# Kernel tuning notes

Hardware: AMD Instinct MI355X
Metric: run time of the kernel (lower is better)

The kernel has to match this reference:

```python
import jax, jax.numpy as jnp
import numpy as np


def setup_inputs() -> dict:
    key = jax.random.key(0)
    ks = jax.random.split(key, 14)
    B, S, C, R = 4, 2048, 1024, 4
    s = 0.02
    inp = {
        "hidden_states": jax.random.normal(ks[0], (B, S, C), jnp.float32),
        "Wq": jax.random.normal(ks[1], (C, C), jnp.float32) * s,
        "Wk": jax.random.normal(ks[2], (C, C), jnp.float32) * s,
        "Wv": jax.random.normal(ks[3], (C, C), jnp.float32) * s,
        "Wo": jax.random.normal(ks[4], (C, C), jnp.float32) * s,
        "bo": jnp.zeros((C,), jnp.float32),
        "q_down": jax.random.normal(ks[5], (R, C), jnp.float32) * (1.0 / R),
        "q_up": jnp.zeros((C, R), jnp.float32) + jax.random.normal(ks[6], (C, R), jnp.float32) * s,
        "k_down": jax.random.normal(ks[7], (R, C), jnp.float32) * (1.0 / R),
        "k_up": jax.random.normal(ks[8], (C, R), jnp.float32) * s,
        "v_down": jax.random.normal(ks[9], (R, C), jnp.float32) * (1.0 / R),
        "v_up": jax.random.normal(ks[10], (C, R), jnp.float32) * s,
        "o_down": jax.random.normal(ks[11], (R, C), jnp.float32) * (1.0 / R),
        "o_up": jax.random.normal(ks[12], (C, R), jnp.float32) * s,
        "num_heads": 16,
    }
    return inp


def _lora_linear(x, W, down, up, scale):
    # base Linear (no bias) + lora_scale * up(down(x))
    base = jnp.einsum("bsc,oc->bso", x, W)
    low = jnp.einsum("bsc,rc->bsr", x, down)
    return base + scale * jnp.einsum("bsr,or->bso", low, up)


def reference(hidden_states, Wq, Wk, Wv, Wo, bo,
              q_down, q_up, k_down, k_up, v_down, v_up, o_down, o_up,
              num_heads):
    B, S, C = hidden_states.shape
    H = num_heads
    D = C // H
    lora_scale = 1.0

    q = _lora_linear(hidden_states, Wq, q_down, q_up, lora_scale)
    k = _lora_linear(hidden_states, Wk, k_down, k_up, lora_scale)
    v = _lora_linear(hidden_states, Wv, v_down, v_up, lora_scale)

    # head_to_batch_dim: [B,S,C] -> [B,H,S,D]
    q = q.reshape(B, S, H, D).transpose(0, 2, 1, 3)
    k = k.reshape(B, S, H, D).transpose(0, 2, 1, 3)
    v = v.reshape(B, S, H, D).transpose(0, 2, 1, 3)

    scale = 1.0 / jnp.sqrt(jnp.asarray(D, hidden_states.dtype))
    scores = jnp.einsum("bhsd,bhtd->bhst", q, k) * scale  # [B,H,S,S]
    probs = jax.nn.softmax(scores, axis=-1)
    out = jnp.einsum("bhst,bhtd->bhsd", probs, v)

    # batch_to_head_dim: [B,H,S,D] -> [B,S,C]
    out = out.transpose(0, 2, 1, 3).reshape(B, S, C)

    out = _lora_linear(out, Wo, o_down, o_up, lora_scale) + bo
    return out
```

## Files before the change

kernel.cpp:

```cpp
#include <hip/hip_runtime.h>
#include <stdint.h>

typedef __attribute__((ext_vector_type(8))) short short8;
typedef __attribute__((ext_vector_type(4))) float f32x4;

typedef const unsigned int __attribute__((address_space(1))) gu32;
typedef unsigned int __attribute__((address_space(3))) lu32;

__device__ __forceinline__ float bf2f(unsigned short u) {
  union { unsigned int i; float f; } v; v.i = ((unsigned int)u) << 16; return v.f;
}
__device__ __forceinline__ unsigned short f2bf(float f) {
  union { float f; unsigned int i; } v; v.f = f;
  unsigned int r = v.i + 0x7FFFu + ((v.i >> 16) & 1u);
  return (unsigned short)(r >> 16);
}
__device__ __forceinline__ float fexp2(float x) {
  float r; asm("v_exp_f32 %0, %1" : "=v"(r) : "v"(x)); return r;
}
__device__ __forceinline__ unsigned int cvtpk(float lo, float hi) {
  unsigned int r;
  asm("v_cvt_pk_bf16_f32 %0, %1, %2" : "=v"(r) : "v"(lo), "v"(hi));
  return r;
}

__global__ __launch_bounds__(256) void fold_w(
    const float* __restrict__ Wq, const float* __restrict__ Wk,
    const float* __restrict__ Wv, const float* __restrict__ Wo,
    const float* __restrict__ qd, const float* __restrict__ qu,
    const float* __restrict__ kd, const float* __restrict__ ku,
    const float* __restrict__ vd, const float* __restrict__ vu,
    const float* __restrict__ od, const float* __restrict__ ou,
    unsigned short* __restrict__ Wqkv, unsigned short* __restrict__ Wob)
{
  int idx = blockIdx.x * 256 + threadIdx.x;
  int sel = idx >> 18;
  int rem = (idx & 0x3FFFF) * 4;
  int o = rem >> 10, c = rem & 1023;
  const float *W, *up, *dn;
  if (sel == 0)      { W = Wq; up = qu; dn = qd; }
  else if (sel == 1) { W = Wk; up = ku; dn = kd; }
  else if (sel == 2) { W = Wv; up = vu; dn = vd; }
  else               { W = Wo; up = ou; dn = od; }
  float4 wv = *(const float4*)&W[rem];
  float a0 = wv.x, a1 = wv.y, a2 = wv.z, a3 = wv.w;
  #pragma unroll
  for (int r = 0; r < 4; r++) {
    float u = up[o * 4 + r];
    float4 dv = *(const float4*)&dn[r * 1024 + c];
    a0 += u * dv.x; a1 += u * dv.y; a2 += u * dv.z; a3 += u * dv.w;
  }
  unsigned long long pk = (unsigned long long)f2bf(a0) |
                          ((unsigned long long)f2bf(a1) << 16) |
                          ((unsigned long long)f2bf(a2) << 32) |
                          ((unsigned long long)f2bf(a3) << 48);
  if (sel < 3) *(unsigned long long*)&Wqkv[sel * 1048576 + rem] = pk;
  else         *(unsigned long long*)&Wob[rem] = pk;
}

__global__ __launch_bounds__(256) void cvt_x(const float* __restrict__ X,
                                             unsigned short* __restrict__ Xb)
{
  int i = (blockIdx.x * 256 + threadIdx.x) * 4;
  float4 v = *(const float4*)&X[i];
  unsigned short o0 = f2bf(v.x), o1 = f2bf(v.y), o2 = f2bf(v.z), o3 = f2bf(v.w);
  unsigned long long pk = (unsigned long long)o0 | ((unsigned long long)o1 << 16) |
                          ((unsigned long long)o2 << 32) | ((unsigned long long)o3 << 48);
  *(unsigned long long*)&Xb[i] = pk;
}

template <int OUTF>
__global__ __launch_bounds__(256) void gemm_bt(
    const unsigned short* __restrict__ A, const unsigned short* __restrict__ B,
    unsigned short* __restrict__ Cb, float* __restrict__ Cf,
    const float* __restrict__ bias, int M, int N, int K)
{
  __shared__ unsigned short smA[3][128 * 32];
  __shared__ unsigned short smB[3][128 * 32];
  const int tid = threadIdx.x;
  const int w = tid >> 6, lane = tid & 63;
  const int g = lane >> 4, lr = lane & 15;
  const int m0 = blockIdx.y * 128, n0 = blockIdx.x * 128;
  const int srow = lane >> 2;
  const int scol = (lane & 3) * 8;
  const unsigned short* gA = A + (size_t)(m0 + w * 16 + srow) * K + scol;
  const unsigned short* gB = B + (size_t)(n0 + w * 16 + srow) * K + scol;
  f32x4 acc[4][4] = {};
  const int wr = (w >> 1) * 64, wc = (w & 1) * 64;

  auto stage = [&](int buf, int k0) {
    #pragma unroll
    for (int i = 0; i < 2; i++) {
      __builtin_amdgcn_global_load_lds((gu32*)(gA + (size_t)i * 64 * K + k0),
          (lu32*)&smA[buf][(i * 64 + w * 16) * 32], 16, 0, 0);
      __builtin_amdgcn_global_load_lds((gu32*)(gB + (size_t)i * 64 * K + k0),
          (lu32*)&smB[buf][(i * 64 + w * 16) * 32], 16, 0, 0);
    }
  };
  auto compute = [&](int buf) {
    short8 a[4], b[4];
    #pragma unroll
    for (int mi = 0; mi < 4; mi++) a[mi] = *(const short8*)&smA[buf][(wr + mi * 16 + lr) * 32 + g * 8];
    #pragma unroll
    for (int ni = 0; ni < 4; ni++) b[ni] = *(const short8*)&smB[buf][(wc + ni * 16 + lr) * 32 + g * 8];
    #pragma unroll
    for (int mi = 0; mi < 4; mi++)
      #pragma unroll
      for (int ni = 0; ni < 4; ni++)
        acc[mi][ni] = __builtin_amdgcn_mfma_f32_16x16x32_bf16(a[mi], b[ni], acc[mi][ni], 0, 0, 0);
  };

  const int nt = K / 32;
  stage(0, 0);
  stage(1, 32);
  int cur = 0;
  for (int t = 0; t + 2 < nt; ++t) {
    asm volatile("s_waitcnt vmcnt(4)" ::: "memory");
    __builtin_amdgcn_sched_barrier(0);
    __builtin_amdgcn_s_barrier();
    __builtin_amdgcn_sched_barrier(0);
    int nb = (cur == 0) ? 2 : cur - 1;
    stage(nb, (t + 2) * 32);
    compute(cur);
    asm volatile("s_waitcnt lgkmcnt(0)" ::: "memory");
    __builtin_amdgcn_sched_barrier(0);
    cur = (cur == 2) ? 0 : cur + 1;
  }
  asm volatile("s_waitcnt vmcnt(4)" ::: "memory");
  __builtin_amdgcn_sched_barrier(0);
  __builtin_amdgcn_s_barrier();
  __builtin_amdgcn_sched_barrier(0);
  compute(cur);
  asm volatile("s_waitcnt lgkmcnt(0)" ::: "memory");
  __builtin_amdgcn_sched_barrier(0);
  cur = (cur == 2) ? 0 : cur + 1;
  asm volatile("s_waitcnt vmcnt(0)" ::: "memory");
  __builtin_amdgcn_sched_barrier(0);
  __builtin_amdgcn_s_barrier();
  __builtin_amdgcn_sched_barrier(0);
  compute(cur);

  #pragma unroll
  for (int mi = 0; mi < 4; mi++) {
    #pragma unroll
    for (int ni = 0; ni < 4; ni++) {
      int col = n0 + wc + ni * 16 + lr;
      #pragma unroll
      for (int j = 0; j < 4; j++) {
        int row = m0 + wr + mi * 16 + g * 4 + j;
        if (OUTF == 0) Cb[(size_t)row * N + col] = f2bf(acc[mi][ni][j]);
        else           Cf[(size_t)row * N + col] = acc[mi][ni][j] + bias[col];
      }
    }
  }
}

__global__ __launch_bounds__(256) void prep_kv(
    const unsigned short* __restrict__ QKV,
    unsigned short* __restrict__ Kswz, unsigned short* __restrict__ VTs)
{
  __shared__ unsigned short vt[64 * 72];
  int bh = blockIdx.x;
  int st = blockIdx.y;
  int b = bh >> 4, h = bh & 15;
  int s0 = st * 64;
  int tid = threadIdx.x;
  #pragma unroll
  for (int i = 0; i < 2; i++) {
    int idx = tid + i * 256;
    int r = idx >> 3, gch = idx & 7;
    size_t rowg = (size_t)(b * 2048 + s0 + r) * 3072;
    short8 kv = *(const short8*)&QKV[rowg + 1024 + h * 64 + gch * 8];
    int gout = gch ^ (r & 7);
    *(short8*)&Kswz[(size_t)(bh * 2048 + s0 + r) * 64 + gout * 8] = kv;
    short8 vv = *(const short8*)&QKV[rowg + 2048 + h * 64 + gch * 8];
    *(short8*)&vt[r * 72 + gch * 8] = vv;
  }
  __syncthreads();
  #pragma unroll
  for (int i = 0; i < 2; i++) {
    int idx = tid + i * 256;
    int d = idx >> 3, gp = idx & 7;
    int gs = gp ^ (d & 7);
    short8 o;
    #pragma unroll
    for (int j = 0; j < 8; j++) o[j] = (short)vt[(gs * 8 + j) * 72 + d];
    *(short8*)&VTs[(size_t)(bh * 64 + d) * 2048 + s0 + gp * 8] = o;
  }
}

__global__ __launch_bounds__(512, 4) void attn(
    const unsigned short* __restrict__ QKV,
    const unsigned short* __restrict__ Kswz,
    const unsigned short* __restrict__ VTs,
    unsigned short* __restrict__ O)
{
  __shared__ unsigned short smK[3][64 * 64];
  __shared__ unsigned short smV[3][64 * 64];
  __shared__ unsigned short smP[8][32 * 64];
  int bh = blockIdx.x, qb = blockIdx.y;
  int b = bh >> 4, h = bh & 15;
  int tid = threadIdx.x, w = tid >> 6, lane = tid & 63;
  int g = lane >> 4, lr = lane & 15;
  int q0 = qb * 256 + w * 32;
  const size_t kbse = (size_t)bh * 2048 * 64;
  const size_t vbse = (size_t)bh * 64 * 2048;
  const int srow8 = lane >> 3;
  const int sc8 = (lane & 7) * 8;

  auto stage = [&](int buf, int n0) {
    const unsigned short* gk = &Kswz[kbse + (size_t)(n0 + w * 8 + srow8) * 64 + sc8];
    __builtin_amdgcn_global_load_lds((gu32*)gk, (lu32*)&smK[buf][(w * 8) * 64], 16, 0, 0);
    const unsigned short* gv = &VTs[vbse + (size_t)(w * 8 + srow8) * 2048 + n0 + sc8];
    __builtin_amdgcn_global_load_lds((gu32*)gv, (lu32*)&smV[buf][(w * 8) * 64], 16, 0, 0);
  };

  const float SC = 0.125f * 1.44269504f;
  short8 bq[2][2];
  #pragma unroll
  for (int qf = 0; qf < 2; qf++)
    #pragma unroll
    for (int ks = 0; ks < 2; ks++) {
      short8 v = *(const short8*)&QKV[(size_t)(b * 2048 + q0 + qf * 16 + lr) * 3072 +
                                      h * 64 + ks * 32 + g * 8];
      #pragma unroll
      for (int j = 0; j < 4; j++) {
        float f0 = bf2f((unsigned short)v[2 * j]) * SC;
        float f1 = bf2f((unsigned short)v[2 * j + 1]) * SC;
        ((unsigned int*)&v)[j] = cvtpk(f0, f1);
      }
      bq[qf][ks] = v;
    }

  short8 vones;
  #pragma unroll
  for (int j = 0; j < 8; j++) vones[j] = (short)0x3F80;

  f32x4 acc_o[2][4] = {};
  f32x4 acc_l[2] = {};

  asm volatile("s_waitcnt vmcnt(0)" ::: "memory");
  __builtin_amdgcn_sched_barrier(0);
  stage(0, 0);
  stage(1, 64);

  auto compute = [&](int buf) {
    const unsigned short* K_ = smK[buf];
    const unsigned short* V_ = smV[buf];
    f32x4 s[4][2] = {};
    __builtin_amdgcn_s_setprio(1);
    #pragma unroll
    for (int nf = 0; nf < 4; nf++) {
      int row = nf * 16 + lr;
      #pragma unroll
      for (int ks = 0; ks < 2; ks++) {
        int eo = (ks * 64 + g * 16) ^ ((row & 7) << 4);
        short8 ak = *(const short8*)&K_[row * 64 + (eo >> 1)];
        #pragma unroll
        for (int qf = 0; qf < 2; qf++)
          s[nf][qf] = __builtin_amdgcn_mfma_f32_16x16x32_bf16(ak, bq[qf][ks], s[nf][qf], 0, 0, 0);
      }
    }
    __builtin_amdgcn_s_setprio(0);

    #pragma unroll
    for (int qf = 0; qf < 2; qf++) {
      int q = qf * 16 + lr;
      #pragma unroll
      for (int nf = 0; nf < 4; nf++) {
        float p0 = fexp2(s[nf][qf][0]);
        float p1 = fexp2(s[nf][qf][1]);
        float p2 = fexp2(s[nf][qf][2]);
        float p3 = fexp2(s[nf][qf][3]);
        uint2 pw;
        pw.x = cvtpk(p0, p1);
        pw.y = cvtpk(p2, p3);
        int eo = ((nf * 16 + g * 4) * 2) ^ ((q & 7) << 4);
        *(uint2*)&smP[w][q * 64 + (eo >> 1)] = pw;
      }
    }

    __builtin_amdgcn_s_setprio(1);
    #pragma unroll
    for (int ks = 0; ks < 2; ks++) {
      short8 ap[2];
      #pragma unroll
      for (int mq = 0; mq < 2; mq++) {
        int q = mq * 16 + lr;
        int eo = (ks * 64 + g * 16) ^ ((q & 7) << 4);
        ap[mq] = *(const short8*)&smP[w][q * 64 + (eo >> 1)];
        acc_l[mq] = __builtin_amdgcn_mfma_f32_16x16x32_bf16(ap[mq], vones, acc_l[mq], 0, 0, 0);
      }
      #pragma unroll
      for (int df = 0; df < 4; df++) {
        int d = df * 16 + lr;
        int eo = (ks * 64 + g * 16) ^ ((d & 7) << 4);
        short8 bv = *(const short8*)&V_[d * 64 + (eo >> 1)];
        #pragma unroll
        for (int mq = 0; mq < 2; mq++)
          acc_o[mq][df] = __builtin_amdgcn_mfma_f32_16x16x32_bf16(ap[mq], bv, acc_o[mq][df], 0, 0, 0);
      }
    }
    __builtin_amdgcn_s_setprio(0);
  };

  int cur = 0;
  for (int t = 0; t + 2 < 32; ++t) {
    asm volatile("s_waitcnt vmcnt(2)" ::: "memory");
    __builtin_amdgcn_sched_barrier(0);
    __builtin_amdgcn_s_barrier();
    __builtin_amdgcn_sched_barrier(0);
    int nb = (cur == 0) ? 2 : cur - 1;
    stage(nb, (t + 2) * 64);
    compute(cur);
    asm volatile("s_waitcnt lgkmcnt(0)" ::: "memory");
    __builtin_amdgcn_sched_barrier(0);
    cur = (cur == 2) ? 0 : cur + 1;
  }
  asm volatile("s_waitcnt vmcnt(2)" ::: "memory");
  __builtin_amdgcn_sched_barrier(0);
  __builtin_amdgcn_s_barrier();
  __builtin_amdgcn_sched_barrier(0);
  compute(cur);
  asm volatile("s_waitcnt lgkmcnt(0)" ::: "memory");
  __builtin_amdgcn_sched_barrier(0);
  cur = (cur == 2) ? 0 : cur + 1;
  asm volatile("s_waitcnt vmcnt(0)" ::: "memory");
  __builtin_amdgcn_sched_barrier(0);
  __builtin_amdgcn_s_barrier();
  __builtin_amdgcn_sched_barrier(0);
  compute(cur);

  #pragma unroll
  for (int mq = 0; mq < 2; mq++)
    #pragma unroll
    for (int j = 0; j < 4; j++) {
      float inv = 1.0f / acc_l[mq][j];
      #pragma unroll
      for (int df = 0; df < 4; df++) {
        int row = b * 2048 + q0 + mq * 16 + g * 4 + j;
        int col = h * 64 + df * 16 + lr;
        O[(size_t)row * 1024 + col] = f2bf(acc_o[mq][df][j] * inv);
      }
    }
}

extern "C" void kernel_launch(void* const* d_in, const int* in_sizes, int n_in,
                              void* d_out, int out_size, void* d_ws, size_t ws_size,
                              hipStream_t stream) {
  const float* X  = (const float*)d_in[0];
  const float* Wq = (const float*)d_in[1];
  const float* Wk = (const float*)d_in[2];
  const float* Wv = (const float*)d_in[3];
  const float* Wo = (const float*)d_in[4];
  const float* bo = (const float*)d_in[5];
  const float* qd = (const float*)d_in[6];
  const float* qu = (const float*)d_in[7];
  const float* kd = (const float*)d_in[8];
  const float* ku = (const float*)d_in[9];
  const float* vd = (const float*)d_in[10];
  const float* vu = (const float*)d_in[11];
  const float* od = (const float*)d_in[12];
  const float* ou = (const float*)d_in[13];

  char* ws = (char*)d_ws;
  unsigned short* Wqkv = (unsigned short*)(ws);
  unsigned short* Wob  = (unsigned short*)(ws + 6291456);
  unsigned short* Xb   = (unsigned short*)(ws + 8388608);
  unsigned short* QKV  = (unsigned short*)(ws + 25165824);
  unsigned short* Kswz = (unsigned short*)(ws + 75497472);
  unsigned short* VTs  = (unsigned short*)(ws + 92274688);

  fold_w<<<4096, 256, 0, stream>>>(Wq, Wk, Wv, Wo, qd, qu, kd, ku, vd, vu, od, ou, Wqkv, Wob);
  cvt_x<<<8192, 256, 0, stream>>>(X, Xb);
  gemm_bt<0><<<dim3(24, 64), 256, 0, stream>>>(Xb, Wqkv, QKV, nullptr, nullptr, 8192, 3072, 1024);
  prep_kv<<<dim3(64, 32), 256, 0, stream>>>(QKV, Kswz, VTs);
  attn<<<dim3(64, 8), 512, 0, stream>>>(QKV, Kswz, VTs, Xb);
  gemm_bt<1><<<dim3(8, 64), 256, 0, stream>>>(Xb, Wob, nullptr, (float*)d_out, bo, 8192, 1024, 1024);
}
```

Before: 193.7 us.

## Fuse K swizzle into QKV GEMM epilogue, enlarge GEMM tiles, merge prep kernels

The X conversion and weight folding now run in a single launch. The QKV GEMM epilogue writes the K section directly in the swizzled per-head layout, so the separate K copy drops out of the prep kernel, which now only transposes V. Both GEMMs move to 256x128 tiles with 512 threads and an XCD-aware 1D block mapping, for better operand reuse and L2 locality. The trade-off is that K is now written as scattered 2-byte stores from the epilogue, and larger tiles mean fewer blocks per GEMM.

```diff
diff --git a/kernel.cpp b/kernel.cpp
--- a/kernel.cpp
+++ b/kernel.cpp
@@ -24,7 +24,8 @@
   return r;
 }
 
-__global__ __launch_bounds__(256) void fold_w(
+__global__ __launch_bounds__(256) void prep_in(
+    const float* __restrict__ X, unsigned short* __restrict__ Xb,
     const float* __restrict__ Wq, const float* __restrict__ Wk,
     const float* __restrict__ Wv, const float* __restrict__ Wo,
     const float* __restrict__ qd, const float* __restrict__ qu,
@@ -33,7 +34,17 @@
     const float* __restrict__ od, const float* __restrict__ ou,
     unsigned short* __restrict__ Wqkv, unsigned short* __restrict__ Wob)
 {
-  int idx = blockIdx.x * 256 + threadIdx.x;
+  if (blockIdx.x < 8192) {
+    int i = (blockIdx.x * 256 + threadIdx.x) * 4;
+    float4 v = *(const float4*)&X[i];
+    unsigned long long pk = (unsigned long long)f2bf(v.x) |
+                            ((unsigned long long)f2bf(v.y) << 16) |
+                            ((unsigned long long)f2bf(v.z) << 32) |
+                            ((unsigned long long)f2bf(v.w) << 48);
+    *(unsigned long long*)&Xb[i] = pk;
+    return;
+  }
+  int idx = (blockIdx.x - 8192) * 256 + threadIdx.x;
   int sel = idx >> 18;
   int rem = (idx & 0x3FFFF) * 4;
   int o = rem >> 10, c = rem & 1023;
@@ -58,44 +69,36 @@
   else         *(unsigned long long*)&Wob[rem] = pk;
 }
 
-__global__ __launch_bounds__(256) void cvt_x(const float* __restrict__ X,
-                                             unsigned short* __restrict__ Xb)
-{
-  int i = (blockIdx.x * 256 + threadIdx.x) * 4;
-  float4 v = *(const float4*)&X[i];
-  unsigned short o0 = f2bf(v.x), o1 = f2bf(v.y), o2 = f2bf(v.z), o3 = f2bf(v.w);
-  unsigned long long pk = (unsigned long long)o0 | ((unsigned long long)o1 << 16) |
-                          ((unsigned long long)o2 << 32) | ((unsigned long long)o3 << 48);
-  *(unsigned long long*)&Xb[i] = pk;
-}
-
 template <int OUTF>
-__global__ __launch_bounds__(256) void gemm_bt(
+__global__ __launch_bounds__(512) void gemm_bt(
     const unsigned short* __restrict__ A, const unsigned short* __restrict__ B,
     unsigned short* __restrict__ Cb, float* __restrict__ Cf,
-    const float* __restrict__ bias, int M, int N, int K)
+    const float* __restrict__ bias, unsigned short* __restrict__ Kswz,
+    int M, int N, int K, int NT, int MCH)
 {
-  __shared__ unsigned short smA[3][128 * 32];
+  __shared__ unsigned short smA[3][256 * 32];
   __shared__ unsigned short smB[3][128 * 32];
   const int tid = threadIdx.x;
   const int w = tid >> 6, lane = tid & 63;
   const int g = lane >> 4, lr = lane & 15;
-  const int m0 = blockIdx.y * 128, n0 = blockIdx.x * 128;
+  const int b1 = blockIdx.x;
+  const int xcd = b1 & 7, idx = b1 >> 3;
+  const int m0 = (xcd * MCH + idx / NT) * 256;
+  const int n0 = (idx % NT) * 128;
   const int srow = lane >> 2;
   const int scol = (lane & 3) * 8;
-  const unsigned short* gA = A + (size_t)(m0 + w * 16 + srow) * K + scol;
+  const unsigned short* gA = A + (size_t)(m0 + w * 32 + srow) * K + scol;
   const unsigned short* gB = B + (size_t)(n0 + w * 16 + srow) * K + scol;
   f32x4 acc[4][4] = {};
   const int wr = (w >> 1) * 64, wc = (w & 1) * 64;
 
   auto stage = [&](int buf, int k0) {
-    #pragma unroll
-    for (int i = 0; i < 2; i++) {
-      __builtin_amdgcn_global_load_lds((gu32*)(gA + (size_t)i * 64 * K + k0),
-          (lu32*)&smA[buf][(i * 64 + w * 16) * 32], 16, 0, 0);
-      __builtin_amdgcn_global_load_lds((gu32*)(gB + (size_t)i * 64 * K + k0),
-          (lu32*)&smB[buf][(i * 64 + w * 16) * 32], 16, 0, 0);
-    }
+    __builtin_amdgcn_global_load_lds((gu32*)(gA + k0),
+        (lu32*)&smA[buf][(w * 32) * 32], 16, 0, 0);
+    __builtin_amdgcn_global_load_lds((gu32*)(gA + (size_t)16 * K + k0),
+        (lu32*)&smA[buf][(w * 32 + 16) * 32], 16, 0, 0);
+    __builtin_amdgcn_global_load_lds((gu32*)(gB + k0),
+        (lu32*)&smB[buf][(w * 16) * 32], 16, 0, 0);
   };
   auto compute = [&](int buf) {
     short8 a[4], b[4];
@@ -115,7 +118,7 @@
   stage(1, 32);
   int cur = 0;
   for (int t = 0; t + 2 < nt; ++t) {
-    asm volatile("s_waitcnt vmcnt(4)" ::: "memory");
+    asm volatile("s_waitcnt vmcnt(3)" ::: "memory");
     __builtin_amdgcn_sched_barrier(0);
     __builtin_amdgcn_s_barrier();
     __builtin_amdgcn_sched_barrier(0);
@@ -126,7 +129,7 @@
     __builtin_amdgcn_sched_barrier(0);
     cur = (cur == 2) ? 0 : cur + 1;
   }
-  asm volatile("s_waitcnt vmcnt(4)" ::: "memory");
+  asm volatile("s_waitcnt vmcnt(3)" ::: "memory");
   __builtin_amdgcn_sched_barrier(0);
   __builtin_amdgcn_s_barrier();
   __builtin_amdgcn_sched_barrier(0);
@@ -145,19 +148,34 @@
     #pragma unroll
     for (int ni = 0; ni < 4; ni++) {
       int col = n0 + wc + ni * 16 + lr;
-      #pragma unroll
-      for (int j = 0; j < 4; j++) {
-        int row = m0 + wr + mi * 16 + g * 4 + j;
-        if (OUTF == 0) Cb[(size_t)row * N + col] = f2bf(acc[mi][ni][j]);
-        else           Cf[(size_t)row * N + col] = acc[mi][ni][j] + bias[col];
-      }
-    }
-  }
-}
-
-__global__ __launch_bounds__(256) void prep_kv(
-    const unsigned short* __restrict__ QKV,
-    unsigned short* __restrict__ Kswz, unsigned short* __restrict__ VTs)
+      if (OUTF == 0) {
+        bool ksec = (Kswz != nullptr) && (n0 + wc + ni * 16) >= 1024 &&
+                    (n0 + wc + ni * 16) < 2048;
+        #pragma unroll
+        for (int j = 0; j < 4; j++) {
+          int row = m0 + wr + mi * 16 + g * 4 + j;
+          unsigned short ov = f2bf(acc[mi][ni][j]);
+          if (ksec) {
+            int b_ = row >> 11, s = row & 2047;
+            int ck = col - 1024, h = ck >> 6, d = ck & 63;
+            Kswz[((size_t)(b_ * 16 + h) * 2048 + s) * 64 + (d ^ ((s & 7) << 3))] = ov;
+          } else {
+            Cb[(size_t)row * N + col] = ov;
+          }
+        }
+      } else {
+        #pragma unroll
+        for (int j = 0; j < 4; j++) {
+          int row = m0 + wr + mi * 16 + g * 4 + j;
+          Cf[(size_t)row * N + col] = acc[mi][ni][j] + bias[col];
+        }
+      }
+    }
+  }
+}
+
+__global__ __launch_bounds__(256) void prep_v(
+    const unsigned short* __restrict__ QKV, unsigned short* __restrict__ VTs)
 {
   __shared__ unsigned short vt[64 * 72];
   int bh = blockIdx.x;
@@ -170,9 +188,6 @@
     int idx = tid + i * 256;
     int r = idx >> 3, gch = idx & 7;
     size_t rowg = (size_t)(b * 2048 + s0 + r) * 3072;
-    short8 kv = *(const short8*)&QKV[rowg + 1024 + h * 64 + gch * 8];
-    int gout = gch ^ (r & 7);
-    *(short8*)&Kswz[(size_t)(bh * 2048 + s0 + r) * 64 + gout * 8] = kv;
     short8 vv = *(const short8*)&QKV[rowg + 2048 + h * 64 + gch * 8];
     *(short8*)&vt[r * 72 + gch * 8] = vv;
   }
@@ -371,10 +386,12 @@
   unsigned short* Kswz = (unsigned short*)(ws + 75497472);
   unsigned short* VTs  = (unsigned short*)(ws + 92274688);
 
-  fold_w<<<4096, 256, 0, stream>>>(Wq, Wk, Wv, Wo, qd, qu, kd, ku, vd, vu, od, ou, Wqkv, Wob);
-  cvt_x<<<8192, 256, 0, stream>>>(X, Xb);
-  gemm_bt<0><<<dim3(24, 64), 256, 0, stream>>>(Xb, Wqkv, QKV, nullptr, nullptr, 8192, 3072, 1024);
-  prep_kv<<<dim3(64, 32), 256, 0, stream>>>(QKV, Kswz, VTs);
+  prep_in<<<12288, 256, 0, stream>>>(X, Xb, Wq, Wk, Wv, Wo, qd, qu, kd, ku,
+                                     vd, vu, od, ou, Wqkv, Wob);
+  gemm_bt<0><<<768, 512, 0, stream>>>(Xb, Wqkv, QKV, nullptr, nullptr, Kswz,
+                                      8192, 3072, 1024, 24, 4);
+  prep_v<<<dim3(64, 32), 256, 0, stream>>>(QKV, VTs);
   attn<<<dim3(64, 8), 512, 0, stream>>>(QKV, Kswz, VTs, Xb);
-  gemm_bt<1><<<dim3(8, 64), 256, 0, stream>>>(Xb, Wob, nullptr, (float*)d_out, bo, 8192, 1024, 1024);
-}
+  gemm_bt<1><<<256, 512, 0, stream>>>(Xb, Wob, nullptr, (float*)d_out, bo,
+                                      nullptr, 8192, 1024, 1024, 8, 4);
+}
```

Result: slower. 229.3 us (+18.4%).
